# Kernel optimization log

Hardware: AMD Instinct MI355X
Metric: run time of the kernel (lower is better)

The kernel has to match this reference:

```python
import jax, jax.numpy as jnp
import numpy as np

B, H, V, L = 4096, 1024, 64, 16  # batch, hidden_size, msg_vocsize, max_msg_len


def setup_inputs() -> dict:
    key = jax.random.key(0)
    ks = jax.random.split(key, 10)
    s = 1.0 / np.sqrt(H)
    return {
        "encoder_hidden": jax.random.normal(ks[0], (B, H), jnp.float32),
        "encoder_cell": jax.random.normal(ks[1], (B, H), jnp.float32),
        "W_ih": jax.random.uniform(ks[2], (4 * H, H), jnp.float32, -s, s),
        "W_hh": jax.random.uniform(ks[3], (4 * H, H), jnp.float32, -s, s),
        "b_ih": jax.random.uniform(ks[4], (4 * H,), jnp.float32, -s, s),
        "b_hh": jax.random.uniform(ks[5], (4 * H,), jnp.float32, -s, s),
        "W_out": jax.random.uniform(ks[6], (V, H), jnp.float32, -s, s),
        "b_out": jax.random.uniform(ks[7], (V,), jnp.float32, -s, s),
        "init_input": jnp.zeros((1, H), jnp.float32),  # nn.Parameter initialized to zeros
        "msg_embedding": jax.random.normal(ks[8], (V, H), jnp.float32),
    }


def reference(encoder_hidden, encoder_cell, W_ih, W_hh, b_ih, b_hh,
              W_out, b_out, init_input, msg_embedding):
    batch = encoder_hidden.shape[0]
    x0 = jnp.broadcast_to(init_input, (batch, H))

    def step(carry, _):
        h, c, x, logp = carry
        x = jax.nn.relu(x)
        gates = x @ W_ih.T + b_ih + h @ W_hh.T + b_hh  # [B, 4H]
        i, f, g, o = jnp.split(gates, 4, axis=-1)      # torch LSTMCell gate order
        i, f, o = jax.nn.sigmoid(i), jax.nn.sigmoid(f), jax.nn.sigmoid(o)
        g = jnp.tanh(g)
        c = f * c + i * g
        h = o * jnp.tanh(c)
        logits = h @ W_out.T + b_out                   # [B, V]
        probs = jax.nn.softmax(logits, axis=1)
        pred = jax.nn.one_hot(jnp.argmax(probs, axis=1), V, dtype=probs.dtype)
        logp = logp + jnp.log(jnp.sum(probs * pred, axis=1))
        x = pred @ msg_embedding                       # [B, H]
        return (h, c, x, logp), (pred, logits)

    init = (encoder_hidden, encoder_cell, x0, jnp.zeros((batch,), encoder_hidden.dtype))
    (_, _, _, log_probs), (message, digits) = jax.lax.scan(step, init, None, length=L)
    mask = jnp.ones((L, 1, batch), encoder_hidden.dtype)
    return message, mask, digits, log_probs
```

## Files before the change

### kernel.cpp

```cpp
#include <hip/hip_runtime.h>
#include <math.h>

#define HD    1024
#define BATCH 4096
#define VOC   64
#define MSGL  16
#define KH    1024
#define NG    4096

typedef _Float16 f16;
typedef _Float16 f16x8 __attribute__((ext_vector_type(8)));
typedef _Float16 f16x4 __attribute__((ext_vector_type(4)));
typedef float    f32x4 __attribute__((ext_vector_type(4)));

__device__ __forceinline__ void splt(float v, f16& hi, f16& lo) {
    f16 h = (f16)v;
    hi = h;
    lo = (f16)(v - (float)h);
}

__device__ __forceinline__ float sigm_f(float x) {
    return __builtin_amdgcn_rcpf(1.0f + __builtin_amdgcn_exp2f(-1.44269504088896f * x));
}
__device__ __forceinline__ float tanh_f(float x) {
    return 1.0f - 2.0f * __builtin_amdgcn_rcpf(1.0f + __builtin_amdgcn_exp2f(2.88539008177793f * x));
}

__device__ __forceinline__ int orig_n(int np) {
    const int bxx = np >> 8, rem = np & 255;
    const int jh = rem >> 6, g = (rem >> 4) & 3, cnn = rem & 15;
    return g * 1024 + bxx * 64 + jh * 16 + cnn;
}
__device__ __forceinline__ int j_of(int np) {
    const int bxx = np >> 8, rem = np & 255;
    const int jh = rem >> 6, cnn = rem & 15;
    return bxx * 64 + jh * 16 + cnn;
}

__device__ __forceinline__ void async16(void* lds, const void* g) {
    __builtin_amdgcn_global_load_lds(
        (const __attribute__((address_space(1))) void*)g,
        (__attribute__((address_space(3))) void*)lds, 16, 0, 0);
}

__device__ __forceinline__ int swz(int row, int gran) {
    return row * 128 + ((gran ^ (row & 7)) << 4);
}

__device__ __forceinline__ void stage(char* ldsbase, const f16* hi, const f16* lo,
                                      int gbase, int k0, int r, int tid) {
    const int o   = (r * 512 + tid) * 16;
    const int row = o >> 7;
    const int gp  = (o >> 4) & 7;
    const int g   = gp ^ (row & 7);
    const f16* src = (g < 4 ? hi : lo) + (size_t)(gbase + row) * KH + k0 + (g & 3) * 8;
    async16(ldsbase + o, src);
}

__global__ __launch_bounds__(512, 1) void gemm_fused(
    const f16* __restrict__ Hh, const f16* __restrict__ Hl,
    const f16* __restrict__ Whi, const f16* __restrict__ Wlo,
    const f16* __restrict__ Wohi, const f16* __restrict__ Wolo,
    const float* __restrict__ XG, const float* __restrict__ b_out,
    float* __restrict__ cbuf,
    f16* __restrict__ HhN, f16* __restrict__ HlN,
    float* __restrict__ omsg0, float* __restrict__ odig0,
    float* __restrict__ ologp, int t)
{
    __shared__ char smem[147456];
    __shared__ int sAm[256];

    const int tid  = threadIdx.x;
    const int lane = tid & 63;
    const int wv   = tid >> 6;
    const int wm   = wv >> 2;
    const int wn   = wv & 3;
    const int bx   = blockIdx.x;
    const int by   = blockIdx.y;
    const int bm   = by * 256;
    const int bnp  = bx * 256;
    const int rl   = lane & 15;
    const int kg   = lane >> 4;

    f32x4 acc[8][4];
    f32x4 acc_l[8];
#pragma unroll
    for (int i = 0; i < 8; ++i) {
#pragma unroll
        for (int g = 0; g < 4; ++g) acc[i][g] = f32x4{0.f, 0.f, 0.f, 0.f};
        acc_l[i] = f32x4{0.f, 0.f, 0.f, 0.f};
    }

#pragma unroll
    for (int r = 0; r < 4; ++r) stage(smem,          Hh,   Hl,   bm,  0, r, tid);
    stage(smem + 131072,                             Wohi, Wolo, 0,   0, 0, tid);
#pragma unroll
    for (int r = 0; r < 4; ++r) stage(smem + 65536,  Whi,  Wlo,  bnp, 0, r, tid);

    for (int kt = 0; kt < 32; ++kt) {
        const char* cb  = smem + (kt & 1) * 32768;
        const char* cbB = smem + 65536 + (kt & 1) * 32768;
        const char* cbW = smem + 131072 + (kt & 1) * 8192;
        char* nb  = smem + ((kt + 1) & 1) * 32768;
        char* nbB = smem + 65536 + ((kt + 1) & 1) * 32768;
        char* nbW = smem + 131072 + ((kt + 1) & 1) * 8192;
        const int kn = ((kt + 1) & 31) * 32;

        asm volatile("s_waitcnt vmcnt(4)" ::: "memory");
        asm volatile("s_barrier" ::: "memory");

#pragma unroll
        for (int r = 0; r < 4; ++r) stage(nb, Hh, Hl, bm, kn, r, tid);
        stage(nbW, Wohi, Wolo, 0, kn, 0, tid);

        asm volatile("s_waitcnt vmcnt(5)" ::: "memory");
        asm volatile("s_barrier" ::: "memory");

        f16x8 bh[4], bl[4];
#pragma unroll
        for (int f = 0; f < 4; ++f) {
            const int row = wn * 64 + f * 16 + rl;
            bh[f] = *(const f16x8*)(cbB + swz(row, kg));
            bl[f] = *(const f16x8*)(cbB + swz(row, kg + 4));
        }
        const f16x8 woh = *(const f16x8*)(cbW + swz(wn * 16 + rl, kg));
        const f16x8 wol = *(const f16x8*)(cbW + swz(wn * 16 + rl, kg + 4));
#pragma unroll
        for (int r = 0; r < 4; ++r) stage(nbB, Whi, Wlo, bnp, kn, r, tid);

        __builtin_amdgcn_s_setprio(1);
#pragma unroll
        for (int f = 0; f < 8; ++f) {
            const int row = wm * 128 + f * 16 + rl;
            const f16x8 ah = *(const f16x8*)(cb + swz(row, kg));
            const f16x8 al = *(const f16x8*)(cb + swz(row, kg + 4));
#pragma unroll
            for (int g = 0; g < 4; ++g) {
                acc[f][g] = __builtin_amdgcn_mfma_f32_16x16x32_f16(ah, bh[g], acc[f][g], 0, 0, 0);
                acc[f][g] = __builtin_amdgcn_mfma_f32_16x16x32_f16(ah, bl[g], acc[f][g], 0, 0, 0);
                acc[f][g] = __builtin_amdgcn_mfma_f32_16x16x32_f16(al, bh[g], acc[f][g], 0, 0, 0);
            }
            acc_l[f] = __builtin_amdgcn_mfma_f32_16x16x32_f16(ah, woh, acc_l[f], 0, 0, 0);
            acc_l[f] = __builtin_amdgcn_mfma_f32_16x16x32_f16(ah, wol, acc_l[f], 0, 0, 0);
            acc_l[f] = __builtin_amdgcn_mfma_f32_16x16x32_f16(al, woh, acc_l[f], 0, 0, 0);
        }
        __builtin_amdgcn_s_setprio(0);
    }

    asm volatile("s_waitcnt vmcnt(0)" ::: "memory");
    __syncthreads();

    const int q = lane >> 4;

    float* sL = (float*)smem;
    if (t > 0) {
        const int ti = t - 1;
        const float bo = b_out[wn * 16 + rl];
#pragma unroll
        for (int f = 0; f < 8; ++f)
#pragma unroll
            for (int rg = 0; rg < 4; ++rg) {
                const int row = wm * 128 + f * 16 + q * 4 + rg;
                sL[row * 65 + wn * 16 + rl] = acc_l[f][rg] + bo;
            }
        __syncthreads();
        if (tid < 256) {
            const int row = tid;
            float m = -1e30f; int am = 0;
#pragma unroll 8
            for (int c = 0; c < 64; ++c) {
                const float v = sL[row * 65 + c];
                if (v > m) { m = v; am = c; }
            }
            float s = 0.f;
#pragma unroll 8
            for (int c = 0; c < 64; ++c)
                s += __builtin_amdgcn_exp2f(1.44269504088896f * (sL[row * 65 + c] - m));
            sAm[row] = am;
            if (bx == 0) {
                const float prev = (ti == 0) ? 0.f : ologp[bm + row];
                ologp[bm + row] = prev - logf(s);
            }
        }
        __syncthreads();
        if (bx == 0) {
            float* omsg = omsg0 + (size_t)ti * BATCH * VOC;
            float* odig = odig0 + (size_t)ti * BATCH * VOC;
#pragma unroll
            for (int i = 0; i < 8; ++i) {
                const int idx = i * 512 + tid;
                const int row = idx >> 6;
                const int c   = idx & 63;
                odig[(size_t)(bm + row) * VOC + c] = sL[row * 65 + c];
                omsg[(size_t)(bm + row) * VOC + c] = (c == sAm[row]) ? 1.0f : 0.0f;
            }
        }
        __syncthreads();
    } else {
        if (tid < 256) sAm[tid] = 64;
        __syncthreads();
    }

    float* sXG = (float*)smem;
    f16*   hHi = (f16*)(smem + 66560);
    f16*   hLo = (f16*)(smem + 99328);
    const int jb = bx * 64;

#pragma unroll
    for (int i = 0; i < 9; ++i) {
        const int idx = i * 512 + tid;
        if (idx < 65 * 64) {
            const int v  = idx >> 6;
            const int c4 = (idx & 63) * 4;
            *(float4*)&sXG[v * 256 + c4] =
                *(const float4*)&XG[(size_t)v * NG + bnp + c4];
        }
    }
    __syncthreads();

    const int lcol = wn * 16 + rl;
    const int jglob = jb + lcol;
#pragma unroll
    for (int i = 0; i < 8; ++i) {
#pragma unroll
        for (int rg = 0; rg < 4; ++rg) {
            const int lrow = wm * 128 + i * 16 + q * 4 + rg;
            const int v = sAm[lrow];
            const float4 xg = *(const float4*)&sXG[v * 256 + lcol * 4];
            const size_t ci = (size_t)(bm + lrow) * HD + jglob;
            const float cold = cbuf[ci];
            const float I = sigm_f(acc[i][0][rg] + xg.x);
            const float F = sigm_f(acc[i][1][rg] + xg.y);
            const float G = tanh_f(acc[i][2][rg] + xg.z);
            const float O = sigm_f(acc[i][3][rg] + xg.w);
            const float cc = F * cold + I * G;
            const float hh = O * tanh_f(cc);
            cbuf[ci] = cc;
            f16 hi_, lo_;
            splt(hh, hi_, lo_);
            hHi[lrow * 64 + lcol] = hi_;
            hLo[lrow * 64 + lcol] = lo_;
        }
    }
    __syncthreads();

#pragma unroll
    for (int r = 0; r < 8; ++r) {
        const int idx = r * 512 + tid;
        const int row = idx >> 4;
        const int c4  = (idx & 15) * 4;
        *(f16x4*)&HhN[(size_t)(bm + row) * HD + jb + c4] = *(f16x4*)&hHi[row * 64 + c4];
        *(f16x4*)&HlN[(size_t)(bm + row) * HD + jb + c4] = *(f16x4*)&hLo[row * 64 + c4];
    }
}

__global__ __launch_bounds__(256) void logits_step(
    const f16* __restrict__ Hh, const f16* __restrict__ Hl,
    const float* __restrict__ W_outT, const float* __restrict__ b_out,
    float* __restrict__ omsg, float* __restrict__ odig,
    float* __restrict__ ologp, int t)
{
    const int lane = threadIdx.x & 63;
    const int wv   = threadIdx.x >> 6;
    const int r0   = blockIdx.x * 8 + wv * 2;

    float a0 = 0.f, a1 = 0.f;
    const f16* hh0 = Hh + (size_t)r0 * HD;
    const f16* hl0 = Hl + (size_t)r0 * HD;
    const f16* hh1 = hh0 + HD;
    const f16* hl1 = hl0 + HD;
    for (int k = 0; k < HD; k += 4) {
        const float w0 = W_outT[(k + 0) * 64 + lane];
        const float w1 = W_outT[(k + 1) * 64 + lane];
        const float w2 = W_outT[(k + 2) * 64 + lane];
        const float w3 = W_outT[(k + 3) * 64 + lane];
        const f16x4 vh0 = *(const f16x4*)&hh0[k];
        const f16x4 vl0 = *(const f16x4*)&hl0[k];
        const f16x4 vh1 = *(const f16x4*)&hh1[k];
        const f16x4 vl1 = *(const f16x4*)&hl1[k];
        a0 += w0 * ((float)vh0[0] + (float)vl0[0]) + w1 * ((float)vh0[1] + (float)vl0[1])
            + w2 * ((float)vh0[2] + (float)vl0[2]) + w3 * ((float)vh0[3] + (float)vl0[3]);
        a1 += w0 * ((float)vh1[0] + (float)vl1[0]) + w1 * ((float)vh1[1] + (float)vl1[1])
            + w2 * ((float)vh1[2] + (float)vl1[2]) + w3 * ((float)vh1[3] + (float)vl1[3]);
    }
    const float bo = b_out[lane];
    const float accs[2] = {a0, a1};

#pragma unroll
    for (int r = 0; r < 2; ++r) {
        const int row = r0 + r;
        const float lg = accs[r] + bo;

        float m = lg; int am = lane;
#pragma unroll
        for (int d = 1; d < 64; d <<= 1) {
            const float om = __shfl_xor(m, d);
            const int   oa = __shfl_xor(am, d);
            if (om > m || (om == m && oa < am)) { m = om; am = oa; }
        }
        float s = expf(lg - m);
#pragma unroll
        for (int d = 1; d < 64; d <<= 1) s += __shfl_xor(s, d);

        odig[(size_t)row * VOC + lane] = lg;
        omsg[(size_t)row * VOC + lane] = (lane == am) ? 1.0f : 0.0f;
        if (lane == 0) {
            const float prev = (t == 0) ? 0.0f : ologp[row];
            ologp[row] = prev - logf(s);
        }
    }
}

__global__ __launch_bounds__(256) void xg_kernel(
    const float* __restrict__ W_ih, const float* __restrict__ rembT,
    const float* __restrict__ rembX0, const float* __restrict__ bR,
    float* __restrict__ XG)
{
    __shared__ float sW[4][1024];
    const int lane = threadIdx.x & 63;
    const int wv   = threadIdx.x >> 6;
    const int np   = blockIdx.x * 4 + wv;
    const int orig = orig_n(np);
    const float* wr = W_ih + (size_t)orig * HD;
#pragma unroll
    for (int c = 0; c < 4; ++c)
        *(float4*)&sW[wv][c * 256 + lane * 4] = *(const float4*)&wr[c * 256 + lane * 4];
    __syncthreads();

    float acc = 0.f, acc0 = 0.f;
#pragma unroll 4
    for (int k = 0; k < HD; ++k) {
        const float w = sW[wv][k];
        acc  += w * rembT[k * 64 + lane];
        acc0 += w * rembX0[k];
    }
    const float b = bR[np];
    const int g = (np >> 4) & 3;
    const int pos = j_of(np) * 4 + g;
    XG[(size_t)lane * NG + pos] = acc + b;
    if (lane == 0) XG[(size_t)64 * NG + pos] = acc0 + b;
}

__global__ __launch_bounds__(256) void prep_all(
    const float* __restrict__ W_hh, const float* __restrict__ ench,
    const float* __restrict__ encc, const float* __restrict__ W_out,
    const float* __restrict__ b_ih, const float* __restrict__ b_hh,
    const float* __restrict__ emb, const float* __restrict__ x0,
    f16* __restrict__ Whi, f16* __restrict__ Wlo,
    f16* __restrict__ Hh, f16* __restrict__ Hl,
    float* __restrict__ cbuf,
    float* __restrict__ W_outT, f16* __restrict__ Wohi, f16* __restrict__ Wolo,
    float* __restrict__ rembT, float* __restrict__ rembX0,
    float* __restrict__ bR, float* __restrict__ mask)
{
    const int u = blockIdx.x * 256 + threadIdx.x;
    const long long idx = (long long)u * 4;

    {
        const int np = (int)(idx >> 10);
        const int k  = (int)(idx & 1023);
        const float4 v = *(const float4*)&W_hh[(size_t)orig_n(np) * HD + k];
        f16x4 vh, vl; f16 hi_, lo_;
        splt(v.x, hi_, lo_); vh[0] = hi_; vl[0] = lo_;
        splt(v.y, hi_, lo_); vh[1] = hi_; vl[1] = lo_;
        splt(v.z, hi_, lo_); vh[2] = hi_; vl[2] = lo_;
        splt(v.w, hi_, lo_); vh[3] = hi_; vl[3] = lo_;
        *(f16x4*)&Whi[idx] = vh;
        *(f16x4*)&Wlo[idx] = vl;
    }
    {
        const float4 v = *(const float4*)&ench[idx];
        f16x4 vh, vl; f16 hi_, lo_;
        splt(v.x, hi_, lo_); vh[0] = hi_; vl[0] = lo_;
        splt(v.y, hi_, lo_); vh[1] = hi_; vl[1] = lo_;
        splt(v.z, hi_, lo_); vh[2] = hi_; vl[2] = lo_;
        splt(v.w, hi_, lo_); vh[3] = hi_; vl[3] = lo_;
        *(f16x4*)&Hh[idx] = vh;
        *(f16x4*)&Hl[idx] = vl;
    }
    *(float4*)&cbuf[idx] = *(const float4*)&encc[idx];

    if (u < 65536) {
        const int i = u;
        mask[i] = 1.0f;
        const int v = i >> 10, k = i & 1023;
        const float wo = W_out[i];
        W_outT[k * 64 + v] = wo;
        f16 hi2, lo2; splt(wo, hi2, lo2);
        Wohi[i] = hi2; Wolo[i] = lo2;
        rembT[k * 64 + v] = fmaxf(emb[i], 0.f);
        if (i < 1024) rembX0[i] = fmaxf(x0[i], 0.f);
        if (i < NG) {
            const int orig = orig_n(i);
            bR[i] = b_ih[orig] + b_hh[orig];
        }
    }
}

extern "C" void kernel_launch(void* const* d_in, const int* in_sizes, int n_in,
                              void* d_out, int out_size, void* d_ws, size_t ws_size,
                              hipStream_t stream)
{
    const float* ench  = (const float*)d_in[0];
    const float* encc  = (const float*)d_in[1];
    const float* W_ih  = (const float*)d_in[2];
    const float* W_hh  = (const float*)d_in[3];
    const float* b_ih  = (const float*)d_in[4];
    const float* b_hh  = (const float*)d_in[5];
    const float* W_out = (const float*)d_in[6];
    const float* b_out = (const float*)d_in[7];
    const float* x0    = (const float*)d_in[8];
    const float* emb   = (const float*)d_in[9];
    float* out = (float*)d_out;

    char* ws = (char*)d_ws;
    f16*   Hh[2]  = { (f16*)(ws + ((size_t) 0 << 20)), (f16*)(ws + ((size_t)16 << 20)) };
    f16*   Hl[2]  = { (f16*)(ws + ((size_t) 8 << 20)), (f16*)(ws + ((size_t)24 << 20)) };
    f16*   Whr    = (f16*)(ws + ((size_t)32 << 20));
    f16*   Wlr    = (f16*)(ws + ((size_t)40 << 20));
    float* cbuf   = (float*)(ws + ((size_t)48 << 20));
    float* W_outT = (float*)(ws + ((size_t)64 << 20));
    float* rembT  = (float*)(ws + ((size_t)65 << 20));
    float* rembX0 = (float*)(ws + ((size_t)66 << 20));
    float* bR     = (float*)(ws + ((size_t)66 << 20) + 8192);
    float* XG     = (float*)(ws + ((size_t)67 << 20));
    f16*   Wohi   = (f16*)(ws + ((size_t)70 << 20));
    f16*   Wolo   = (f16*)(ws + ((size_t)71 << 20));

    float* out_msg0 = out;
    float* out_mask = out + (size_t)MSGL * BATCH * VOC;
    float* out_dig0 = out_mask + (size_t)MSGL * BATCH;
    float* out_logp = out_dig0 + (size_t)MSGL * BATCH * VOC;

    prep_all<<<4096, 256, 0, stream>>>(
        W_hh, ench, encc, W_out, b_ih, b_hh, emb, x0,
        Whr, Wlr, Hh[0], Hl[0], cbuf,
        W_outT, Wohi, Wolo, rembT, rembX0, bR, out_mask);
    xg_kernel<<<1024, 256, 0, stream>>>(W_ih, rembT, rembX0, bR, XG);

    for (int t = 0; t < MSGL; ++t) {
        const int cur = t & 1, nxt = cur ^ 1;
        gemm_fused<<<dim3(16, 16), 512, 0, stream>>>(
            Hh[cur], Hl[cur], Whr, Wlr, Wohi, Wolo, XG, b_out,
            cbuf, Hh[nxt], Hl[nxt],
            out_msg0, out_dig0, out_logp, t);
    }
    logits_step<<<512, 256, 0, stream>>>(
        Hh[0], Hl[0], W_outT, b_out,
        out_msg0 + (size_t)(MSGL - 1) * BATCH * VOC,
        out_dig0 + (size_t)(MSGL - 1) * BATCH * VOC,
        out_logp, MSGL - 1);
}
```

Before: 1.942 ms.

## Interleave next-tile staging with MFMA sub-phases in the LSTM gate GEMM loop

Splits each k-iteration into four sub-phases that each load two A fragments, issue part of the next tile's global-to-LDS staging, and run the corresponding MFMAs. The goal is to spread memory traffic across the compute instead of bunching all staging at the start behind two waits and barriers. Waits are placed at finer points so that B and W_out buffers become ready earlier. In exchange it adds more barriers per iteration, and the hand-tuned vmcnt counts must match the number of loads each stage issues.

```diff
diff --git a/kernel.cpp b/kernel.cpp
--- a/kernel.cpp
+++ b/kernel.cpp
@@ -91,60 +91,86 @@
         acc_l[i] = f32x4{0.f, 0.f, 0.f, 0.f};
     }
 
-#pragma unroll
-    for (int r = 0; r < 4; ++r) stage(smem,          Hh,   Hl,   bm,  0, r, tid);
-    stage(smem + 131072,                             Wohi, Wolo, 0,   0, 0, tid);
-#pragma unroll
-    for (int r = 0; r < 4; ++r) stage(smem + 65536,  Whi,  Wlo,  bnp, 0, r, tid);
+    stage(smem + 65536,  Whi,  Wlo,  bnp, 0, 0, tid);
+    stage(smem + 65536,  Whi,  Wlo,  bnp, 0, 1, tid);
+    stage(smem + 131072, Wohi, Wolo, 0,   0, 0, tid);
+    stage(smem + 65536,  Whi,  Wlo,  bnp, 0, 2, tid);
+    stage(smem + 65536,  Whi,  Wlo,  bnp, 0, 3, tid);
+    stage(smem,          Hh,   Hl,   bm,  0, 0, tid);
+    stage(smem,          Hh,   Hl,   bm,  0, 2, tid);
+    stage(smem,          Hh,   Hl,   bm,  0, 1, tid);
+    stage(smem,          Hh,   Hl,   bm,  0, 3, tid);
+    asm volatile("s_waitcnt vmcnt(2)" ::: "memory");
+    asm volatile("s_barrier" ::: "memory");
 
     for (int kt = 0; kt < 32; ++kt) {
-        const char* cb  = smem + (kt & 1) * 32768;
+        const char* cbA = smem + (kt & 1) * 32768;
         const char* cbB = smem + 65536 + (kt & 1) * 32768;
         const char* cbW = smem + 131072 + (kt & 1) * 8192;
-        char* nb  = smem + ((kt + 1) & 1) * 32768;
+        char* nbA = smem + ((kt + 1) & 1) * 32768;
         char* nbB = smem + 65536 + ((kt + 1) & 1) * 32768;
         char* nbW = smem + 131072 + ((kt + 1) & 1) * 8192;
         const int kn = ((kt + 1) & 31) * 32;
 
-        asm volatile("s_waitcnt vmcnt(4)" ::: "memory");
-        asm volatile("s_barrier" ::: "memory");
-
-#pragma unroll
-        for (int r = 0; r < 4; ++r) stage(nb, Hh, Hl, bm, kn, r, tid);
-        stage(nbW, Wohi, Wolo, 0, kn, 0, tid);
-
-        asm volatile("s_waitcnt vmcnt(5)" ::: "memory");
-        asm volatile("s_barrier" ::: "memory");
-
-        f16x8 bh[4], bl[4];
-#pragma unroll
-        for (int f = 0; f < 4; ++f) {
-            const int row = wn * 64 + f * 16 + rl;
-            bh[f] = *(const f16x8*)(cbB + swz(row, kg));
-            bl[f] = *(const f16x8*)(cbB + swz(row, kg + 4));
-        }
-        const f16x8 woh = *(const f16x8*)(cbW + swz(wn * 16 + rl, kg));
-        const f16x8 wol = *(const f16x8*)(cbW + swz(wn * 16 + rl, kg + 4));
-#pragma unroll
-        for (int r = 0; r < 4; ++r) stage(nbB, Whi, Wlo, bnp, kn, r, tid);
-
-        __builtin_amdgcn_s_setprio(1);
-#pragma unroll
-        for (int f = 0; f < 8; ++f) {
-            const int row = wm * 128 + f * 16 + rl;
-            const f16x8 ah = *(const f16x8*)(cb + swz(row, kg));
-            const f16x8 al = *(const f16x8*)(cb + swz(row, kg + 4));
-#pragma unroll
-            for (int g = 0; g < 4; ++g) {
-                acc[f][g] = __builtin_amdgcn_mfma_f32_16x16x32_f16(ah, bh[g], acc[f][g], 0, 0, 0);
-                acc[f][g] = __builtin_amdgcn_mfma_f32_16x16x32_f16(ah, bl[g], acc[f][g], 0, 0, 0);
-                acc[f][g] = __builtin_amdgcn_mfma_f32_16x16x32_f16(al, bh[g], acc[f][g], 0, 0, 0);
-            }
-            acc_l[f] = __builtin_amdgcn_mfma_f32_16x16x32_f16(ah, woh, acc_l[f], 0, 0, 0);
-            acc_l[f] = __builtin_amdgcn_mfma_f32_16x16x32_f16(ah, wol, acc_l[f], 0, 0, 0);
-            acc_l[f] = __builtin_amdgcn_mfma_f32_16x16x32_f16(al, woh, acc_l[f], 0, 0, 0);
-        }
-        __builtin_amdgcn_s_setprio(0);
+        f16x8 bh[4], bl[4], woh, wol;
+
+#pragma unroll
+        for (int q = 0; q < 4; ++q) {
+            f16x8 ah[2], al[2];
+#pragma unroll
+            for (int i = 0; i < 2; ++i) {
+                const int row = wm * 128 + (2 * q + i) * 16 + rl;
+                ah[i] = *(const f16x8*)(cbA + swz(row, kg));
+                al[i] = *(const f16x8*)(cbA + swz(row, kg + 4));
+            }
+            if (q == 0) {
+#pragma unroll
+                for (int g = 0; g < 4; ++g) {
+                    const int row = wn * 64 + g * 16 + rl;
+                    bh[g] = *(const f16x8*)(cbB + swz(row, kg));
+                    bl[g] = *(const f16x8*)(cbB + swz(row, kg + 4));
+                }
+                woh = *(const f16x8*)(cbW + swz(wn * 16 + rl, kg));
+                wol = *(const f16x8*)(cbW + swz(wn * 16 + rl, kg + 4));
+            }
+
+            if (q == 0) {
+                stage(nbB, Whi, Wlo, bnp, kn, 0, tid);
+                stage(nbB, Whi, Wlo, bnp, kn, 1, tid);
+                stage(nbW, Wohi, Wolo, 0, kn, 0, tid);
+            } else if (q == 1) {
+                stage(nbB, Whi, Wlo, bnp, kn, 2, tid);
+                stage(nbB, Whi, Wlo, bnp, kn, 3, tid);
+            } else if (q == 2) {
+                stage(nbA, Hh, Hl, bm, kn, 0, tid);
+                stage(nbA, Hh, Hl, bm, kn, 2, tid);
+            } else {
+                stage(nbA, Hh, Hl, bm, kn, 1, tid);
+                stage(nbA, Hh, Hl, bm, kn, 3, tid);
+            }
+
+            asm volatile("s_barrier" ::: "memory");
+
+            __builtin_amdgcn_s_setprio(1);
+#pragma unroll
+            for (int i = 0; i < 2; ++i) {
+                const int f = 2 * q + i;
+#pragma unroll
+                for (int g = 0; g < 4; ++g) {
+                    acc[f][g] = __builtin_amdgcn_mfma_f32_16x16x32_f16(ah[i], bh[g], acc[f][g], 0, 0, 0);
+                    acc[f][g] = __builtin_amdgcn_mfma_f32_16x16x32_f16(ah[i], bl[g], acc[f][g], 0, 0, 0);
+                    acc[f][g] = __builtin_amdgcn_mfma_f32_16x16x32_f16(al[i], bh[g], acc[f][g], 0, 0, 0);
+                }
+                acc_l[f] = __builtin_amdgcn_mfma_f32_16x16x32_f16(ah[i], woh, acc_l[f], 0, 0, 0);
+                acc_l[f] = __builtin_amdgcn_mfma_f32_16x16x32_f16(ah[i], wol, acc_l[f], 0, 0, 0);
+                acc_l[f] = __builtin_amdgcn_mfma_f32_16x16x32_f16(al[i], woh, acc_l[f], 0, 0, 0);
+            }
+            __builtin_amdgcn_s_setprio(0);
+
+            if (q == 1) asm volatile("s_waitcnt vmcnt(5)" ::: "memory");
+            if (q == 3) asm volatile("s_waitcnt vmcnt(2)" ::: "memory");
+            asm volatile("s_barrier" ::: "memory");
+        }
     }
 
     asm volatile("s_waitcnt vmcnt(0)" ::: "memory");
```

Result: no change. 1.915 ms (-1.3%).
